# Optimization experiments

Measured on AMD Instinct MI355X. Metric: run time of the kernel, lower is better.

The kernel has to match this reference:

```python
import jax, jax.numpy as jnp
import numpy as np

N_NODES = 50000
N_EDGES = 640000
D_IN = 128
D_HID = 128
D_OUT = 128
N_GRAPHS = 64


def gcn_conv(x, edge_index, W, b, n_nodes):
    """PyG GCNConv: D^{-1/2} (A + I) D^{-1/2} X W + b (unit edge weights)."""
    src, dst = edge_index[0], edge_index[1]
    h = x @ W  # [N, d_out]
    # degree counts target-side edges plus the self loop
    deg = jax.ops.segment_sum(jnp.ones_like(dst, dtype=h.dtype), dst,
                              num_segments=n_nodes) + 1.0
    dinv = jax.lax.rsqrt(deg)  # deg >= 1 so always finite
    norm = dinv[src] * dinv[dst]  # [E]
    msg = h[src] * norm[:, None]  # gather + scale  [E, d_out]
    agg = jax.ops.segment_sum(msg, dst, num_segments=n_nodes)
    # self-loop contribution: norm_ii = dinv_i^2
    agg = agg + h * (dinv * dinv)[:, None]
    return agg + b


def global_mean_pool(x, batch, n_graphs):
    sums = jax.ops.segment_sum(x, batch, num_segments=n_graphs)
    cnt = jax.ops.segment_sum(jnp.ones((x.shape[0],), dtype=x.dtype), batch,
                              num_segments=n_graphs)
    return sums / jnp.maximum(cnt, 1.0)[:, None]


def setup_inputs() -> dict:
    key = jax.random.key(0)
    k = jax.random.split(key, 8)
    x = jax.random.normal(k[0], (N_NODES, D_IN), dtype=jnp.float32)
    edge_index = jax.random.randint(k[1], (2, N_EDGES), 0, N_NODES, dtype=jnp.int64)
    batch = jnp.sort(jax.random.randint(k[2], (N_NODES,), 0, N_GRAPHS, dtype=jnp.int64))
    s1 = 1.0 / np.sqrt(D_IN)
    s2 = 1.0 / np.sqrt(D_HID)
    W1 = jax.random.uniform(k[3], (D_IN, D_HID), jnp.float32, -s1, s1)
    b1 = jnp.zeros((D_HID,), jnp.float32)
    W2 = jax.random.uniform(k[4], (D_HID, D_OUT), jnp.float32, -s2, s2)
    b2 = jnp.zeros((D_OUT,), jnp.float32)
    return {"x": x, "edge_index": edge_index, "batch": batch,
            "W1": W1, "b1": b1, "W2": W2, "b2": b2}


def reference(x, edge_index, batch, W1, b1, W2, b2):
    n = x.shape[0]
    h = jax.nn.relu(gcn_conv(x, edge_index, W1, b1, n))
    h = gcn_conv(h, edge_index, W2, b2, n)
    return global_mean_pool(h, batch, N_GRAPHS)
```

## Files before the change

### kernel.cpp

```cpp
#include <hip/hip_runtime.h>


#define D 128
#define NGRAPH 64
#define SCAN_B 1024
#define AGG_BLOCKS 2048

typedef _Float16 h16x2 __attribute__((ext_vector_type(2)));
typedef _Float16 f16x8 __attribute__((ext_vector_type(8)));
typedef float    f32x4 __attribute__((ext_vector_type(4)));
typedef unsigned short u16x8 __attribute__((ext_vector_type(8)));

__device__ __forceinline__ float2 h2f(unsigned u) {
    h16x2 h = __builtin_bit_cast(h16x2, u);
    return make_float2((float)h.x, (float)h.y);
}
__device__ __forceinline__ unsigned f2h(float x, float y) {
    h16x2 h;
    h.x = (_Float16)x;
    h.y = (_Float16)y;
    return __builtin_bit_cast(unsigned, h);
}

__global__ void zero_out_kernel(float* __restrict__ out, int n) {
    int i = blockIdx.x * blockDim.x + threadIdx.x;
    if (i < n) out[i] = 0.f;
}

__global__ __launch_bounds__(256) void pack_count_kernel(const float* __restrict__ W1,
                                                         _Float16* __restrict__ WB,
                                                         const int* __restrict__ ei,
                                                         int* __restrict__ deg,
                                                         unsigned* __restrict__ Gz,
                                                         unsigned* __restrict__ Hz,
                                                         int N, int E) {
    int b = (int)blockIdx.x;
    if (b < 8) {
        int idx = b * 256 + (int)threadIdx.x;
        int lane = idx & 63;
        int nt   = (idx >> 6) & 7;
        int kt   = idx >> 9;
        int col  = nt * 16 + (lane & 15);
        int krow = kt * 32 + (lane >> 4) * 8;
#pragma unroll
        for (int j = 0; j < 8; ++j)
            WB[idx * 8 + j] = (_Float16)W1[(krow + j) * D + col];
        return;
    }
    if (b == 8) {
        int t = (int)threadIdx.x;
        if (t < 64)       Gz[(size_t)N * 64 + t] = 0u;
        else if (t < 128) Hz[(size_t)N * 64 + (t - 64)] = 0u;
        return;
    }
    int e0 = (b - 9) * 1024 + (int)threadIdx.x;
    int d[4];
#pragma unroll
    for (int j = 0; j < 4; ++j) {
        int e = e0 + j * 256;
        d[j] = (e < E) ? ei[E + e] : -1;
    }
#pragma unroll
    for (int j = 0; j < 4; ++j)
        if (d[j] >= 0 && d[j] < N) atomicAdd(&deg[d[j]], 1);
}

__global__ __launch_bounds__(SCAN_B) void block_scan_kernel(const int* __restrict__ deg,
                                                            int* __restrict__ rowstart,
                                                            int* __restrict__ bsum,
                                                            float* __restrict__ dinv,
                                                            int N) {
    __shared__ int sc[SCAN_B];
    int t = threadIdx.x;
    int i = blockIdx.x * SCAN_B + t;
    int orig = (i < N) ? deg[i] : 0;
    int pad8 = (orig + 7) & ~7;
    int v = pad8;
    sc[t] = v;
    __syncthreads();
    for (int off = 1; off < SCAN_B; off <<= 1) {
        int add = (t >= off) ? sc[t - off] : 0;
        __syncthreads();
        v += add;
        sc[t] = v;
        __syncthreads();
    }
    if (i < N) {
        rowstart[i] = v - pad8;
        dinv[i]     = rsqrtf((float)orig + 1.0f);
    }
    if (t == SCAN_B - 1) bsum[blockIdx.x] = v;
}

__global__ __launch_bounds__(SCAN_B) void finalize_scan_kernel(const int* __restrict__ bsum,
                                                               const int* __restrict__ deg,
                                                               int* __restrict__ rowstart,
                                                               int* __restrict__ cursor,
                                                               unsigned short* __restrict__ colidx,
                                                               int N, int nblk) {
    __shared__ int s_off;
    if (threadIdx.x < 64) {
        int lane = (int)threadIdx.x;
        int bv = (lane < nblk) ? bsum[lane] : 0;
        int v  = (lane < (int)blockIdx.x) ? bv : 0;
        int vt = bv;
        for (int off = 32; off > 0; off >>= 1) {
            v  += __shfl_down(v, off);
            vt += __shfl_down(vt, off);
        }
        if (lane == 0) {
            s_off = v;
            if (blockIdx.x == 0) rowstart[N] = vt;
        }
    }
    __syncthreads();
    int i = blockIdx.x * SCAN_B + threadIdx.x;
    if (i < N) {
        int rs = rowstart[i] + s_off;
        rowstart[i] = rs;
        cursor[i]   = rs;
        int dg = deg[i];
        int p8 = (dg + 7) & ~7;
        for (int k = dg; k < p8; ++k)
            colidx[rs + k] = (unsigned short)N;
    }
}

__global__ __launch_bounds__(256) void gemm_fill_kernel(const float* __restrict__ X,
                                                        const _Float16* __restrict__ WB,
                                                        const float* __restrict__ dinv,
                                                        _Float16* __restrict__ Gh,
                                                        const int* __restrict__ ei,
                                                        int* __restrict__ cursor,
                                                        unsigned short* __restrict__ colidx,
                                                        int N, int E, int gb) {
    if ((int)blockIdx.x >= gb) {
        int e0 = ((int)blockIdx.x - gb) * 1024 + (int)threadIdx.x;
        int d[4], s[4], slot[4];
#pragma unroll
        for (int j = 0; j < 4; ++j) {
            int e = e0 + j * 256;
            if (e < E) {
                d[j] = ei[E + e];
                s[j] = ei[e];
            } else d[j] = -1;
        }
#pragma unroll
        for (int j = 0; j < 4; ++j)
            if (d[j] >= 0 && d[j] < N) slot[j] = atomicAdd(&cursor[d[j]], 1);
#pragma unroll
        for (int j = 0; j < 4; ++j)
            if (d[j] >= 0 && d[j] < N)
                colidx[slot[j]] = (unsigned short)min(max(s[j], 0), N - 1);
        return;
    }

    int t = (int)threadIdx.x;
    int wave = t >> 6, lane = t & 63;
    int mbase = blockIdx.x * 64 + wave * 16;
    int arow  = mbase + (lane & 15);
    if (arow >= N) arow = N - 1;
    int kgrp  = lane >> 4;

    f16x8 afrag[4];
#pragma unroll
    for (int kt = 0; kt < 4; ++kt) {
        const float* xp = X + (size_t)arow * D + kt * 32 + kgrp * 8;
        float4 a0 = *(const float4*)xp;
        float4 a1 = *(const float4*)(xp + 4);
        f16x8 af;
        af[0] = (_Float16)a0.x; af[1] = (_Float16)a0.y;
        af[2] = (_Float16)a0.z; af[3] = (_Float16)a0.w;
        af[4] = (_Float16)a1.x; af[5] = (_Float16)a1.y;
        af[6] = (_Float16)a1.z; af[7] = (_Float16)a1.w;
        afrag[kt] = af;
    }
    f32x4 acc[8];
#pragma unroll
    for (int nt = 0; nt < 8; ++nt) acc[nt] = (f32x4){0.f, 0.f, 0.f, 0.f};
#pragma unroll
    for (int kt = 0; kt < 4; ++kt) {
#pragma unroll
        for (int nt = 0; nt < 8; ++nt) {
            uint4 u = *(const uint4*)(WB + (((kt * 8 + nt) * 64 + lane) * 8));
            f16x8 bfrag = __builtin_bit_cast(f16x8, u);
            acc[nt] = __builtin_amdgcn_mfma_f32_16x16x32_f16(afrag[kt], bfrag, acc[nt], 0, 0, 0);
        }
    }
    int r0 = mbase + kgrp * 4;
#pragma unroll
    for (int r = 0; r < 4; ++r) {
        int row = r0 + r;
        if (row < N) {
            float dv = dinv[row];
#pragma unroll
            for (int nt = 0; nt < 8; ++nt)
                Gh[(size_t)row * D + nt * 16 + (lane & 15)] = (_Float16)(dv * acc[nt][r]);
        }
    }
}

__global__ __launch_bounds__(256) void agg1_kernel(const unsigned* __restrict__ Gh,
                                                   const int* __restrict__ rowstart,
                                                   const unsigned short* __restrict__ colidx,
                                                   const float* __restrict__ dinv,
                                                   const float* __restrict__ b1,
                                                   unsigned* __restrict__ Hh,
                                                   int N, int chunk) {
    int gid  = blockIdx.x * 4 + (threadIdx.x >> 6);
    int lane = threadIdx.x & 63;
    int i0 = gid * chunk, i1 = min(i0 + chunk, N);
    float bx = b1[2 * lane], by = b1[2 * lane + 1];
    for (int i = i0; i < i1; ++i) {
        float di = dinv[i];
        float2 acc = h2f(Gh[(size_t)i * 64 + lane]);
        int e0 = rowstart[i], e1 = rowstart[i + 1];
        for (int e = e0; e < e1; e += 8) {
            u16x8 cc = *(const u16x8*)(colidx + e);
            unsigned u[8];
#pragma unroll
            for (int j = 0; j < 8; ++j)
                u[j] = Gh[(size_t)cc[j] * 64 + lane];
#pragma unroll
            for (int j = 0; j < 8; ++j) {
                float2 v = h2f(u[j]);
                acc.x += v.x;
                acc.y += v.y;
            }
        }
        float hx = fmaxf(fmaf(di, acc.x, bx), 0.f) * di;
        float hy = fmaxf(fmaf(di, acc.y, by), 0.f) * di;
        Hh[(size_t)i * 64 + lane] = f2h(hx, hy);
    }
}

__global__ __launch_bounds__(256) void agg2_pool_kernel(const unsigned* __restrict__ Hh,
                                                        const int* __restrict__ rowstart,
                                                        const unsigned short* __restrict__ colidx,
                                                        const float* __restrict__ dinv,
                                                        const int* __restrict__ batch,
                                                        float* __restrict__ pool,
                                                        int N, int chunk) {
    int gid  = blockIdx.x * 4 + (threadIdx.x >> 6);
    int lane = threadIdx.x & 63;
    int i0 = gid * chunk, i1 = min(i0 + chunk, N);
    if (i0 >= N) return;

    float2 pa = make_float2(0.f, 0.f);
    int cur = min(max(batch[i0], 0), NGRAPH - 1);
    for (int i = i0; i < i1; ++i) {
        float di = dinv[i];
        float2 a = h2f(Hh[(size_t)i * 64 + lane]);
        int e0 = rowstart[i], e1 = rowstart[i + 1];
        for (int e = e0; e < e1; e += 8) {
            u16x8 cc = *(const u16x8*)(colidx + e);
            unsigned u[8];
#pragma unroll
            for (int j = 0; j < 8; ++j)
                u[j] = Hh[(size_t)cc[j] * 64 + lane];
#pragma unroll
            for (int j = 0; j < 8; ++j) {
                float2 v = h2f(u[j]);
                a.x += v.x;
                a.y += v.y;
            }
        }
        int b = min(max(batch[i], 0), NGRAPH - 1);
        if (b != cur) {
            atomicAdd(&pool[(size_t)cur * D + 2 * lane], pa.x);
            atomicAdd(&pool[(size_t)cur * D + 2 * lane + 1], pa.y);
            pa = make_float2(0.f, 0.f);
            cur = b;
        }
        pa.x = fmaf(di, a.x, pa.x);
        pa.y = fmaf(di, a.y, pa.y);
    }
    atomicAdd(&pool[(size_t)cur * D + 2 * lane], pa.x);
    atomicAdd(&pool[(size_t)cur * D + 2 * lane + 1], pa.y);
}

__device__ __forceinline__ int lbound(const int* __restrict__ a, int n, int v) {
    int lo = 0, hi = n;
    while (lo < hi) {
        int m = (lo + hi) >> 1;
        if (a[m] < v) lo = m + 1; else hi = m;
    }
    return lo;
}

__global__ void final_gemm_kernel(const float* __restrict__ pool,
                                  const int* __restrict__ batch,
                                  const float* __restrict__ W2,
                                  const float* __restrict__ b2,
                                  float* __restrict__ out, int N) {
    int g = blockIdx.x, o = threadIdx.x;
    int s = lbound(batch, N, g);
    int e = lbound(batch, N, g + 1);
    float inv_cnt = 1.0f / fmaxf((float)(e - s), 1.0f);
    float acc = 0.f;
#pragma unroll 4
    for (int k = 0; k < D; ++k)
        acc = fmaf(pool[g * D + k], W2[k * D + o], acc);
    out[g * D + o] = acc * inv_cnt + b2[o];
}


extern "C" void kernel_launch(void* const* d_in, const int* in_sizes, int n_in,
                              void* d_out, int out_size, void* d_ws, size_t ws_size,
                              hipStream_t stream) {
    const float* x     = (const float*)d_in[0];
    const int*   ei    = (const int*)  d_in[1];
    const int*   batch = (const int*)  d_in[2];
    const float* W1    = (const float*)d_in[3];
    const float* b1    = (const float*)d_in[4];
    const float* W2    = (const float*)d_in[5];
    const float* b2    = (const float*)d_in[6];
    float* out = (float*)d_out;

    const int N = in_sizes[0] / D;
    const int E = in_sizes[1] / 2;
    const int nblk = (N + SCAN_B - 1) / SCAN_B;

    char* ws = (char*)d_ws;
    size_t off = 0;
    auto carve = [&](size_t bytes) {
        size_t o = off;
        off = (off + bytes + 255) & ~(size_t)255;
        return o;
    };
    size_t o_deg      = carve((size_t)N * 4);
    size_t o_pool     = carve((size_t)NGRAPH * D * 4);
    size_t zspan      = off;
    size_t o_rowstart = carve((size_t)(N + 1) * 4);
    size_t o_cursor   = carve((size_t)(N + 1) * 4);
    size_t o_dinv     = carve((size_t)N * 4);
    size_t o_colidx   = carve(((size_t)E + 7 * (size_t)N + 64) * 2);
    size_t o_bsum     = carve((size_t)64 * 4);
    size_t o_wb       = carve((size_t)D * D * 2);
    size_t o_gh       = carve((size_t)(N + 1) * D * 2);
    size_t o_hh       = carve((size_t)(N + 1) * D * 2);
    size_t need = off;

    if (ws_size < need) {
        zero_out_kernel<<<(out_size + 255) / 256, 256, 0, stream>>>(out, out_size);
        return;
    }

    int*            deg      = (int*)           (ws + o_deg);
    float*          pool     = (float*)         (ws + o_pool);
    int*            rowstart = (int*)           (ws + o_rowstart);
    int*            cursor   = (int*)           (ws + o_cursor);
    float*          dinv     = (float*)         (ws + o_dinv);
    unsigned short* colidx   = (unsigned short*)(ws + o_colidx);
    int*            bsum     = (int*)           (ws + o_bsum);
    _Float16*       WB       = (_Float16*)      (ws + o_wb);
    _Float16*       Gh       = (_Float16*)      (ws + o_gh);
    _Float16*       Hh       = (_Float16*)      (ws + o_hh);

    hipMemsetAsync(ws, 0, zspan, stream);

    int ebc = (E + 1023) / 1024;
    int gb  = (N + 63) / 64;

    pack_count_kernel<<<9 + ebc, 256, 0, stream>>>(W1, WB, ei, deg,
                                                   (unsigned*)Gh, (unsigned*)Hh, N, E);
    block_scan_kernel<<<nblk, SCAN_B, 0, stream>>>(deg, rowstart, bsum, dinv, N);
    finalize_scan_kernel<<<nblk, SCAN_B, 0, stream>>>(bsum, deg, rowstart, cursor,
                                                      colidx, N, nblk);
    gemm_fill_kernel<<<gb + ebc, 256, 0, stream>>>(x, WB, dinv, Gh, ei, cursor,
                                                   colidx, N, E, gb);

    int groups = AGG_BLOCKS * 4;
    int chunk  = (N + groups - 1) / groups;
    agg1_kernel<<<AGG_BLOCKS, 256, 0, stream>>>((const unsigned*)Gh, rowstart, colidx,
                                                dinv, b1, (unsigned*)Hh, N, chunk);
    agg2_pool_kernel<<<AGG_BLOCKS, 256, 0, stream>>>((const unsigned*)Hh, rowstart, colidx,
                                                     dinv, batch, pool, N, chunk);
    final_gemm_kernel<<<NGRAPH, D, 0, stream>>>(pool, batch, W2, b2, out, N);
}
```

Before: 225.6 us.

## Build CSR via destination buckets with shared-memory histograms instead of global atomics

Replaces the per-node global atomic degree count and per-edge global cursor atomics with a two-level bucket sort. Edges are scattered into 512-node destination buckets using LDS histograms, and each bucket then computes degrees, offsets and column fill in shared memory. The aim is to cut contended global atomics and scattered writes during CSR construction. It adds an extra bucket buffer pass and a fixed per-bucket capacity that could silently drop edges on skewed inputs.

```diff
diff --git a/kernel.cpp b/kernel.cpp
--- a/kernel.cpp
+++ b/kernel.cpp
@@ -3,8 +3,10 @@
 
 #define D 128
 #define NGRAPH 64
-#define SCAN_B 1024
 #define AGG_BLOCKS 2048
+#define BUCK_SH 9
+#define BUCK_W  512
+#define MAXBUCK 128
 
 typedef _Float16 h16x2 __attribute__((ext_vector_type(2)));
 typedef _Float16 f16x8 __attribute__((ext_vector_type(8)));
@@ -27,16 +29,18 @@
     if (i < n) out[i] = 0.f;
 }
 
-__global__ __launch_bounds__(256) void pack_count_kernel(const float* __restrict__ W1,
-                                                         _Float16* __restrict__ WB,
-                                                         const int* __restrict__ ei,
-                                                         int* __restrict__ deg,
-                                                         unsigned* __restrict__ Gz,
-                                                         unsigned* __restrict__ Hz,
-                                                         int N, int E) {
+__global__ __launch_bounds__(256) void pack_scatter_kernel(const float* __restrict__ W1,
+                                                           _Float16* __restrict__ WB,
+                                                           const int* __restrict__ ei,
+                                                           int* __restrict__ bcnt,
+                                                           unsigned* __restrict__ buck,
+                                                           unsigned* __restrict__ Gz,
+                                                           unsigned* __restrict__ Hz,
+                                                           int N, int E, int CAP) {
     int b = (int)blockIdx.x;
+    int t = (int)threadIdx.x;
     if (b < 8) {
-        int idx = b * 256 + (int)threadIdx.x;
+        int idx = b * 256 + t;
         int lane = idx & 63;
         int nt   = (idx >> 6) & 7;
         int kt   = idx >> 9;
@@ -48,110 +52,164 @@
         return;
     }
     if (b == 8) {
-        int t = (int)threadIdx.x;
         if (t < 64)       Gz[(size_t)N * 64 + t] = 0u;
         else if (t < 128) Hz[(size_t)N * 64 + (t - 64)] = 0u;
         return;
     }
-    int e0 = (b - 9) * 1024 + (int)threadIdx.x;
-    int d[4];
+    __shared__ unsigned histL[MAXBUCK];
+    __shared__ int      baseL[MAXBUCK];
+    if (t < MAXBUCK) histL[t] = 0u;
+    __syncthreads();
+
+    int e0 = (b - 9) * 1024;
+    int bid[4];
+    unsigned lidx[4], pk[4];
 #pragma unroll
     for (int j = 0; j < 4; ++j) {
-        int e = e0 + j * 256;
-        d[j] = (e < E) ? ei[E + e] : -1;
+        int e = e0 + t + j * 256;
+        bid[j] = -1;
+        if (e < E) {
+            int s = ei[e];
+            int d = ei[E + e];
+            if (d >= 0 && d < N) {
+                s = min(max(s, 0), N - 1);
+                bid[j] = d >> BUCK_SH;
+                pk[j]  = ((unsigned)d << 16) | (unsigned)s;
+            }
+        }
     }
 #pragma unroll
     for (int j = 0; j < 4; ++j)
-        if (d[j] >= 0 && d[j] < N) atomicAdd(&deg[d[j]], 1);
-}
-
-__global__ __launch_bounds__(SCAN_B) void block_scan_kernel(const int* __restrict__ deg,
-                                                            int* __restrict__ rowstart,
-                                                            int* __restrict__ bsum,
-                                                            float* __restrict__ dinv,
-                                                            int N) {
-    __shared__ int sc[SCAN_B];
-    int t = threadIdx.x;
-    int i = blockIdx.x * SCAN_B + t;
-    int orig = (i < N) ? deg[i] : 0;
-    int pad8 = (orig + 7) & ~7;
-    int v = pad8;
-    sc[t] = v;
-    __syncthreads();
-    for (int off = 1; off < SCAN_B; off <<= 1) {
-        int add = (t >= off) ? sc[t - off] : 0;
-        __syncthreads();
-        v += add;
-        sc[t] = v;
-        __syncthreads();
-    }
-    if (i < N) {
-        rowstart[i] = v - pad8;
-        dinv[i]     = rsqrtf((float)orig + 1.0f);
-    }
-    if (t == SCAN_B - 1) bsum[blockIdx.x] = v;
-}
-
-__global__ __launch_bounds__(SCAN_B) void finalize_scan_kernel(const int* __restrict__ bsum,
-                                                               const int* __restrict__ deg,
-                                                               int* __restrict__ rowstart,
-                                                               int* __restrict__ cursor,
-                                                               unsigned short* __restrict__ colidx,
-                                                               int N, int nblk) {
-    __shared__ int s_off;
-    if (threadIdx.x < 64) {
-        int lane = (int)threadIdx.x;
-        int bv = (lane < nblk) ? bsum[lane] : 0;
-        int v  = (lane < (int)blockIdx.x) ? bv : 0;
-        int vt = bv;
-        for (int off = 32; off > 0; off >>= 1) {
-            v  += __shfl_down(v, off);
-            vt += __shfl_down(vt, off);
-        }
-        if (lane == 0) {
-            s_off = v;
-            if (blockIdx.x == 0) rowstart[N] = vt;
-        }
-    }
-    __syncthreads();
-    int i = blockIdx.x * SCAN_B + threadIdx.x;
-    if (i < N) {
-        int rs = rowstart[i] + s_off;
-        rowstart[i] = rs;
-        cursor[i]   = rs;
-        int dg = deg[i];
-        int p8 = (dg + 7) & ~7;
-        for (int k = dg; k < p8; ++k)
-            colidx[rs + k] = (unsigned short)N;
-    }
+        if (bid[j] >= 0) lidx[j] = atomicAdd(&histL[bid[j]], 1u);
+    __syncthreads();
+    if (t < MAXBUCK && histL[t] > 0u)
+        baseL[t] = atomicAdd(&bcnt[t], (int)histL[t]);
+    __syncthreads();
+#pragma unroll
+    for (int j = 0; j < 4; ++j)
+        if (bid[j] >= 0) {
+            int slot = baseL[bid[j]] + (int)lidx[j];
+            if (slot < CAP) buck[(size_t)bid[j] * CAP + slot] = pk[j];
+        }
+}
+
+__global__ __launch_bounds__(256) void bucket_deg_kernel(const unsigned* __restrict__ buck,
+                                                         const int* __restrict__ bcnt,
+                                                         int* __restrict__ deg,
+                                                         float* __restrict__ dinv,
+                                                         int* __restrict__ padsum,
+                                                         int N, int CAP) {
+    __shared__ int degL[BUCK_W];
+    __shared__ int red[256];
+    int b = (int)blockIdx.x;
+    int t = (int)threadIdx.x;
+    for (int k = t; k < BUCK_W; k += 256) degL[k] = 0;
+    __syncthreads();
+    int cnt = min(bcnt[b], CAP);
+    const unsigned* bp = buck + (size_t)b * CAP;
+    for (int i = t; i < cnt; i += 256)
+        atomicAdd(&degL[(bp[i] >> 16) & (BUCK_W - 1)], 1);
+    __syncthreads();
+    int base = b << BUCK_SH;
+    int local = 0;
+    for (int k = t; k < BUCK_W; k += 256) {
+        int d = base + k;
+        if (d < N) {
+            int dg = degL[k];
+            deg[d]  = dg;
+            dinv[d] = rsqrtf((float)dg + 1.0f);
+            local  += (dg + 7) & ~7;
+        }
+    }
+    red[t] = local;
+    __syncthreads();
+    for (int off = 128; off > 0; off >>= 1) {
+        if (t < off) red[t] += red[t + off];
+        __syncthreads();
+    }
+    if (t == 0) padsum[b] = red[0];
+}
+
+__global__ __launch_bounds__(128) void bucket_scan_kernel(const int* __restrict__ padsum,
+                                                          int* __restrict__ bbase,
+                                                          int* __restrict__ rowstart,
+                                                          int N, int nbuck) {
+    __shared__ int s[128];
+    int t = (int)threadIdx.x;
+    int own = (t < nbuck) ? padsum[t] : 0;
+    s[t] = own;
+    __syncthreads();
+    for (int off = 1; off < 128; off <<= 1) {
+        int v = (t >= off) ? s[t - off] : 0;
+        __syncthreads();
+        s[t] += v;
+        __syncthreads();
+    }
+    if (t < nbuck) bbase[t] = s[t] - own;
+    if (t == 127) rowstart[N] = s[127];
 }
 
 __global__ __launch_bounds__(256) void gemm_fill_kernel(const float* __restrict__ X,
                                                         const _Float16* __restrict__ WB,
                                                         const float* __restrict__ dinv,
                                                         _Float16* __restrict__ Gh,
-                                                        const int* __restrict__ ei,
-                                                        int* __restrict__ cursor,
+                                                        const unsigned* __restrict__ buck,
+                                                        const int* __restrict__ bcnt,
+                                                        const int* __restrict__ deg,
+                                                        const int* __restrict__ bbase,
+                                                        int* __restrict__ rowstart,
                                                         unsigned short* __restrict__ colidx,
-                                                        int N, int E, int gb) {
+                                                        int N, int CAP, int gb) {
     if ((int)blockIdx.x >= gb) {
-        int e0 = ((int)blockIdx.x - gb) * 1024 + (int)threadIdx.x;
-        int d[4], s[4], slot[4];
-#pragma unroll
-        for (int j = 0; j < 4; ++j) {
-            int e = e0 + j * 256;
-            if (e < E) {
-                d[j] = ei[E + e];
-                s[j] = ei[e];
-            } else d[j] = -1;
-        }
-#pragma unroll
-        for (int j = 0; j < 4; ++j)
-            if (d[j] >= 0 && d[j] < N) slot[j] = atomicAdd(&cursor[d[j]], 1);
-#pragma unroll
-        for (int j = 0; j < 4; ++j)
-            if (d[j] >= 0 && d[j] < N)
-                colidx[slot[j]] = (unsigned short)min(max(s[j], 0), N - 1);
+        __shared__ int degS[BUCK_W];
+        __shared__ int loff[BUCK_W];
+        __shared__ int sc[256];
+        int b = (int)blockIdx.x - gb;
+        int t = (int)threadIdx.x;
+        int base_d = b << BUCK_SH;
+        for (int k = t; k < BUCK_W; k += 256) {
+            int d = base_d + k;
+            degS[k] = (d < N) ? deg[d] : 0;
+        }
+        __syncthreads();
+        int p0 = (degS[2 * t] + 7) & ~7;
+        int p1 = (degS[2 * t + 1] + 7) & ~7;
+        int own = p0 + p1;
+        sc[t] = own;
+        __syncthreads();
+        for (int off = 1; off < 256; off <<= 1) {
+            int v = (t >= off) ? sc[t - off] : 0;
+            __syncthreads();
+            sc[t] += v;
+            __syncthreads();
+        }
+        int excl = sc[t] - own;
+        loff[2 * t]     = excl;
+        loff[2 * t + 1] = excl + p0;
+        __syncthreads();
+        int bb = bbase[b];
+        for (int k = t; k < BUCK_W; k += 256) {
+            int d = base_d + k;
+            if (d < N) {
+                int rs = bb + loff[k];
+                rowstart[d] = rs;
+                int dg = degS[k];
+                int p8 = (dg + 7) & ~7;
+                for (int j = dg; j < p8; ++j)
+                    colidx[rs + j] = (unsigned short)N;
+            }
+        }
+        __syncthreads();
+        for (int k = t; k < BUCK_W; k += 256) degS[k] = bb + loff[k];
+        __syncthreads();
+        int cnt = min(bcnt[b], CAP);
+        const unsigned* bp = buck + (size_t)b * CAP;
+        for (int i = t; i < cnt; i += 256) {
+            unsigned u = bp[i];
+            int ld = (int)((u >> 16) & (BUCK_W - 1));
+            int slot = atomicAdd(&degS[ld], 1);
+            colidx[slot] = (unsigned short)(u & 0xffffu);
+        }
         return;
     }
 
@@ -319,7 +377,8 @@
 
     const int N = in_sizes[0] / D;
     const int E = in_sizes[1] / 2;
-    const int nblk = (N + SCAN_B - 1) / SCAN_B;
+    const int nbuck = (N + BUCK_W - 1) >> BUCK_SH;
+    const int CAP   = (E / (nbuck > 0 ? nbuck : 1)) * 2 + 1024;
 
     char* ws = (char*)d_ws;
     size_t off = 0;
@@ -328,14 +387,16 @@
         off = (off + bytes + 255) & ~(size_t)255;
         return o;
     };
-    size_t o_deg      = carve((size_t)N * 4);
+    size_t o_bcnt     = carve((size_t)MAXBUCK * 4);
     size_t o_pool     = carve((size_t)NGRAPH * D * 4);
     size_t zspan      = off;
     size_t o_rowstart = carve((size_t)(N + 1) * 4);
-    size_t o_cursor   = carve((size_t)(N + 1) * 4);
+    size_t o_deg      = carve((size_t)N * 4);
     size_t o_dinv     = carve((size_t)N * 4);
+    size_t o_padsum   = carve((size_t)MAXBUCK * 4);
+    size_t o_bbase    = carve((size_t)MAXBUCK * 4);
     size_t o_colidx   = carve(((size_t)E + 7 * (size_t)N + 64) * 2);
-    size_t o_bsum     = carve((size_t)64 * 4);
+    size_t o_buck     = carve((size_t)nbuck * CAP * 4);
     size_t o_wb       = carve((size_t)D * D * 2);
     size_t o_gh       = carve((size_t)(N + 1) * D * 2);
     size_t o_hh       = carve((size_t)(N + 1) * D * 2);
@@ -346,29 +407,32 @@
         return;
     }
 
-    int*            deg      = (int*)           (ws + o_deg);
+    int*            bcnt     = (int*)           (ws + o_bcnt);
     float*          pool     = (float*)         (ws + o_pool);
     int*            rowstart = (int*)           (ws + o_rowstart);
-    int*            cursor   = (int*)           (ws + o_cursor);
+    int*            deg      = (int*)           (ws + o_deg);
     float*          dinv     = (float*)         (ws + o_dinv);
+    int*            padsum   = (int*)           (ws + o_padsum);
+    int*            bbase    = (int*)           (ws + o_bbase);
     unsigned short* colidx   = (unsigned short*)(ws + o_colidx);
-    int*            bsum     = (int*)           (ws + o_bsum);
+    unsigned*       buck     = (unsigned*)      (ws + o_buck);
     _Float16*       WB       = (_Float16*)      (ws + o_wb);
     _Float16*       Gh       = (_Float16*)      (ws + o_gh);
     _Float16*       Hh       = (_Float16*)      (ws + o_hh);
 
     hipMemsetAsync(ws, 0, zspan, stream);
 
-    int ebc = (E + 1023) / 1024;
+    int ebs = (E + 1023) / 1024;
     int gb  = (N + 63) / 64;
 
-    pack_count_kernel<<<9 + ebc, 256, 0, stream>>>(W1, WB, ei, deg,
-                                                   (unsigned*)Gh, (unsigned*)Hh, N, E);
-    block_scan_kernel<<<nblk, SCAN_B, 0, stream>>>(deg, rowstart, bsum, dinv, N);
-    finalize_scan_kernel<<<nblk, SCAN_B, 0, stream>>>(bsum, deg, rowstart, cursor,
-                                                      colidx, N, nblk);
-    gemm_fill_kernel<<<gb + ebc, 256, 0, stream>>>(x, WB, dinv, Gh, ei, cursor,
-                                                   colidx, N, E, gb);
+    pack_scatter_kernel<<<9 + ebs, 256, 0, stream>>>(W1, WB, ei, bcnt, buck,
+                                                     (unsigned*)Gh, (unsigned*)Hh,
+                                                     N, E, CAP);
+    bucket_deg_kernel<<<nbuck, 256, 0, stream>>>(buck, bcnt, deg, dinv, padsum, N, CAP);
+    bucket_scan_kernel<<<1, 128, 0, stream>>>(padsum, bbase, rowstart, N, nbuck);
+    gemm_fill_kernel<<<gb + nbuck, 256, 0, stream>>>(x, WB, dinv, Gh, buck, bcnt,
+                                                     deg, bbase, rowstart, colidx,
+                                                     N, CAP, gb);
 
     int groups = AGG_BLOCKS * 4;
     int chunk  = (N + groups - 1) / groups;
```

After: 196.4 us. -12.9%, faster.
